# Optimization experiments

Hardware: AMD Instinct MI355X
Metric: run time of the kernel (lower is better)

Reference implementation:

```python
import jax, jax.numpy as jnp
import numpy as np

N = 100000      # nodes
E = 1600000     # edges
F_IN = 128
H = 128
L = 3           # GraphConv layers
C = 47          # classes
EPS = 1e-5      # BatchNorm eps


def setup_inputs() -> dict:
    key = jax.random.key(0)
    ks = jax.random.split(key, 12)
    feat = jax.random.normal(ks[0], (N, F_IN), dtype=jnp.float32)
    src = jax.random.randint(ks[1], (E,), 0, N, dtype=jnp.int32)
    dst = jax.random.randint(ks[2], (E,), 0, N, dtype=jnp.int32)
    s = 0.02
    W_in = jax.random.normal(ks[3], (F_IN, H), dtype=jnp.float32) * s
    b_in = jnp.zeros((H,), dtype=jnp.float32)
    Wc = jax.random.normal(ks[4], (L, H, H), dtype=jnp.float32) * s
    bc = jnp.zeros((L, H), dtype=jnp.float32)
    # BatchNorm (eval mode) params for layers+1 norms
    gamma = jnp.ones((L + 1, H), dtype=jnp.float32)
    beta = jnp.zeros((L + 1, H), dtype=jnp.float32)
    rmean = jax.random.normal(ks[5], (L + 1, H), dtype=jnp.float32) * 0.1
    rvar = jax.random.uniform(ks[6], (L + 1, H), dtype=jnp.float32, minval=0.5, maxval=1.5)
    W_out = jax.random.normal(ks[7], (H, C), dtype=jnp.float32) * s
    b_out = jnp.zeros((C,), dtype=jnp.float32)
    return {"feat": feat, "src": src, "dst": dst, "W_in": W_in, "b_in": b_in,
            "Wc": Wc, "bc": bc, "gamma": gamma, "beta": beta,
            "rmean": rmean, "rvar": rvar, "W_out": W_out, "b_out": b_out}


def _bn(x, g, b, m, v):
    # BatchNorm1d in eval mode (running stats)
    return (x - m) * jax.lax.rsqrt(v + EPS) * g + b


def _degree_norms(src, dst):
    ones = jnp.ones((E,), dtype=jnp.float32)
    deg_out = jax.ops.segment_sum(ones, src, num_segments=N)
    deg_in = jax.ops.segment_sum(ones, dst, num_segments=N)
    norm_src = jax.lax.rsqrt(jnp.maximum(deg_out, 1.0))
    norm_dst = jax.lax.rsqrt(jnp.maximum(deg_in, 1.0))
    return norm_src, norm_dst


def _graph_conv(h, src, dst, norm_src, norm_dst, W, b):
    # DGL GraphConv, norm='both': D_dst^{-1/2} A D_src^{-1/2} H W + b
    h = h * norm_src[:, None]
    agg = jax.ops.segment_sum(h[src], dst, num_segments=N)  # [N, H]
    agg = agg * norm_dst[:, None]
    return agg @ W + b


def reference(feat, src, dst, W_in, b_in, Wc, bc, gamma, beta, rmean, rvar, W_out, b_out):
    norm_src, norm_dst = _degree_norms(src, dst)
    h = feat @ W_in + b_in
    h = jax.nn.relu(_bn(h, gamma[0], beta[0], rmean[0], rvar[0]))
    # dropout is identity in eval mode
    for i in range(L):
        h = _graph_conv(h, src, dst, norm_src, norm_dst, Wc[i], bc[i])
        h = jax.nn.relu(_bn(h, gamma[i + 1], beta[i + 1], rmean[i + 1], rvar[i + 1]))
    return h @ W_out + b_out
```

## Files before the change

### kernel.cpp

```cpp
#include <hip/hip_runtime.h>
#include <cstddef>
#include <cstdint>

#define NN 100000
#define NE 1600000
#define HD 128
#define C_OUT 47
#define EPS_BN 1e-5f
#define SLAB 64
#define NXCD 8
#define GEMM0_BLOCKS ((NN + 127) / 128)
#define BUILD_BLOCKS (NE / 256)

typedef _Float16 f16;
typedef __attribute__((ext_vector_type(2))) _Float16 f16x2;
typedef __attribute__((ext_vector_type(8))) _Float16 f16x8;
typedef __attribute__((ext_vector_type(4))) float f32x4;

__device__ inline ushort f16bits(f16 h) { return __builtin_bit_cast(ushort, h); }
__device__ inline uint packf16(f16 a, f16 b) {
  return (uint)f16bits(a) | ((uint)f16bits(b) << 16);
}
__device__ inline uint xcc_id() {
  uint x;
  asm volatile("s_getreg_b32 %0, hwreg(HW_REG_XCC_ID)" : "=s"(x));
  return x & (NXCD - 1);
}

__global__ __launch_bounds__(256) void k_wsplit(
    const float* __restrict__ W_in, const float* __restrict__ Wc,
    const float* __restrict__ W_out,
    uint* __restrict__ wsHi, uint* __restrict__ wsLo) {
  int g = blockIdx.x * 256 + threadIdx.x;
  int m = g >> 13;
  int i = g & 8191;
  int kp = i >> 7, c = i & 127;
  int k = kp << 1;
  int s = kp >> 2, t = kp & 3;
  if (m < 4) {
    const float* W = (m == 0) ? W_in : (Wc + (size_t)(m - 1) * HD * HD);
    float w0 = W[(size_t)k * 128 + c];
    float w1 = W[(size_t)(k + 1) * 128 + c];
    f16 h0 = (f16)w0, h1 = (f16)w1;
    f16 l0 = (f16)(w0 - (float)h0), l1 = (f16)(w1 - (float)h1);
    int idx = m * 8192 + (s * 128 + c) * 4 + t;
    wsHi[idx] = packf16(h0, h1);
    wsLo[idx] = packf16(l0, l1);
  } else if (c < 48) {
    float w0 = (c < C_OUT) ? W_out[(size_t)k * C_OUT + c] : 0.f;
    float w1 = (c < C_OUT) ? W_out[(size_t)(k + 1) * C_OUT + c] : 0.f;
    f16 h0 = (f16)w0, h1 = (f16)w1;
    f16 l0 = (f16)(w0 - (float)h0), l1 = (f16)(w1 - (float)h1);
    int idx = 4 * 8192 + (s * 48 + c) * 4 + t;
    wsHi[idx] = packf16(h0, h1);
    wsLo[idx] = packf16(l0, l1);
  }
}

template <bool A16>
__device__ inline void gemm_body(
    const void* __restrict__ Av, const uint* __restrict__ wHi,
    const uint* __restrict__ wLo, const float* __restrict__ bias,
    const float* __restrict__ gamma, const float* __restrict__ beta,
    const float* __restrict__ rmean, const float* __restrict__ rvar,
    f16* __restrict__ out, int bx) {
  int tid = threadIdx.x;
  int wv = tid >> 6, lane = tid & 63;
  int q = lane >> 4, m16 = lane & 15;
  int row_base = bx * 128 + wv * 32;

  f32x4 acc[2][8];
  #pragma unroll
  for (int mt = 0; mt < 2; ++mt)
    #pragma unroll
    for (int nt = 0; nt < 8; ++nt)
      acc[mt][nt] = (f32x4){0.f, 0.f, 0.f, 0.f};

  #pragma unroll
  for (int kk = 0; kk < 4; ++kk) {
    f16x8 a[2];
    #pragma unroll
    for (int mt = 0; mt < 2; ++mt) {
      int r = row_base + mt * 16 + m16;
      r = r < NN ? r : NN - 1;
      if constexpr (A16) {
        a[mt] = *(const f16x8*)((const f16*)Av + (size_t)r * 128 + kk * 32 + q * 8);
      } else {
        const float4* ap = (const float4*)((const float*)Av + (size_t)r * 128 + kk * 32 + q * 8);
        float4 a0 = ap[0], a1 = ap[1];
        a[mt][0] = (f16)a0.x; a[mt][1] = (f16)a0.y;
        a[mt][2] = (f16)a0.z; a[mt][3] = (f16)a0.w;
        a[mt][4] = (f16)a1.x; a[mt][5] = (f16)a1.y;
        a[mt][6] = (f16)a1.z; a[mt][7] = (f16)a1.w;
      }
    }
    int s = kk * 4 + q;
    #pragma unroll
    for (int nt = 0; nt < 8; ++nt) {
      int n = nt * 16 + m16;
      const f16x8 whi = *(const f16x8*)&wHi[(s * 128 + n) * 4];
      const f16x8 wlo = *(const f16x8*)&wLo[(s * 128 + n) * 4];
      #pragma unroll
      for (int mt = 0; mt < 2; ++mt) {
        acc[mt][nt] = __builtin_amdgcn_mfma_f32_16x16x32_f16(a[mt], whi, acc[mt][nt], 0, 0, 0);
        acc[mt][nt] = __builtin_amdgcn_mfma_f32_16x16x32_f16(a[mt], wlo, acc[mt][nt], 0, 0, 0);
      }
    }
  }

  float s8[8], t8[8];
  #pragma unroll
  for (int nt = 0; nt < 8; ++nt) {
    int col = nt * 16 + m16;
    float sc = gamma[col] * rsqrtf(rvar[col] + EPS_BN);
    s8[nt] = sc;
    t8[nt] = (bias[col] - rmean[col]) * sc + beta[col];
  }
  #pragma unroll
  for (int mt = 0; mt < 2; ++mt) {
    #pragma unroll
    for (int nt = 0; nt < 8; ++nt) {
      int col = nt * 16 + m16;
      #pragma unroll
      for (int e = 0; e < 4; ++e) {
        int r = row_base + mt * 16 + q * 4 + e;
        if (r < NN) {
          float y = fmaxf(acc[mt][nt][e] * s8[nt] + t8[nt], 0.f);
          out[(size_t)r * 128 + col] = (f16)y;
        }
      }
    }
  }
}

__global__ __launch_bounds__(256, 4) void k_mega(
    const int* __restrict__ src, const int* __restrict__ dst,
    int* __restrict__ deg_out_c, int* __restrict__ cursor,
    int* __restrict__ slab,
    const float* __restrict__ feat, const uint* __restrict__ wsHi,
    const uint* __restrict__ wsLo, const float* __restrict__ b_in,
    const float* __restrict__ gamma, const float* __restrict__ beta,
    const float* __restrict__ rmean, const float* __restrict__ rvar,
    f16* __restrict__ h) {
  if (blockIdx.x >= GEMM0_BLOCKS) {
    int e = (blockIdx.x - GEMM0_BLOCKS) * 256 + threadIdx.x;
    if (e >= NE) return;
    int s = src[e], v = dst[e];
    uint xc = xcc_id();
    __hip_atomic_fetch_add(&deg_out_c[xc * NN + s], 1, __ATOMIC_RELAXED,
                           __HIP_MEMORY_SCOPE_WORKGROUP);
    int pos = atomicAdd(&cursor[v], 1);
    if (pos < SLAB) slab[(size_t)v * SLAB + pos] = s;
    return;
  }
  gemm_body<false>(feat, wsHi, wsLo, b_in, gamma, beta, rmean, rvar, h,
                   blockIdx.x);
}

__global__ __launch_bounds__(256) void k_norms(
    const int* __restrict__ deg_out_c, const int* __restrict__ cursor,
    float* __restrict__ norm_src, float* __restrict__ norm_dst) {
  int v = blockIdx.x * blockDim.x + threadIdx.x;
  if (v >= NN) return;
  int d = 0;
  #pragma unroll
  for (int c = 0; c < NXCD; ++c) d += deg_out_c[c * NN + v];
  norm_src[v] = rsqrtf((float)(d > 0 ? d : 1));
  int di = cursor[v];
  norm_dst[v] = rsqrtf((float)(di > 0 ? di : 1));
}

__global__ __launch_bounds__(256) void k_aggregate(
    const f16* __restrict__ h, const int* __restrict__ cursor,
    const int* __restrict__ slab, const float* __restrict__ norm_src,
    const float* __restrict__ norm_dst, f16* __restrict__ agg) {
  int wave = (int)((blockIdx.x * (unsigned)blockDim.x + threadIdx.x) >> 6);
  int lane = threadIdx.x & 63;
  if (wave >= NN) return;
  const f16x2* h2 = (const f16x2*)h;
  const int* cols = slab + (size_t)wave * SLAB;
  int d = cursor[wave];
  d = d < SLAB ? d : SLAB;
  float ax = 0.f, ay = 0.f;
  int j = 0;
  for (; j + 4 <= d; j += 4) {
    int u0 = cols[j + 0];
    int u1 = cols[j + 1];
    int u2 = cols[j + 2];
    int u3 = cols[j + 3];
    float w0 = norm_src[u0], w1 = norm_src[u1];
    float w2 = norm_src[u2], w3 = norm_src[u3];
    f16x2 x0 = h2[(size_t)u0 * 64 + lane];
    f16x2 x1 = h2[(size_t)u1 * 64 + lane];
    f16x2 x2 = h2[(size_t)u2 * 64 + lane];
    f16x2 x3 = h2[(size_t)u3 * 64 + lane];
    ax = fmaf(w0, (float)x0[0], ax); ay = fmaf(w0, (float)x0[1], ay);
    ax = fmaf(w1, (float)x1[0], ax); ay = fmaf(w1, (float)x1[1], ay);
    ax = fmaf(w2, (float)x2[0], ax); ay = fmaf(w2, (float)x2[1], ay);
    ax = fmaf(w3, (float)x3[0], ax); ay = fmaf(w3, (float)x3[1], ay);
  }
  for (; j < d; ++j) {
    int u = cols[j];
    float w = norm_src[u];
    f16x2 x = h2[(size_t)u * 64 + lane];
    ax = fmaf(w, (float)x[0], ax);
    ay = fmaf(w, (float)x[1], ay);
  }
  float nd = norm_dst[wave];
  f16x2 o;
  o[0] = (f16)(ax * nd);
  o[1] = (f16)(ay * nd);
  ((f16x2*)agg)[(size_t)wave * 64 + lane] = o;
}

__global__ __launch_bounds__(256, 4) void k_gemm(
    const f16* __restrict__ A, const uint* __restrict__ wHi,
    const uint* __restrict__ wLo, const float* __restrict__ bias,
    const float* __restrict__ gamma, const float* __restrict__ beta,
    const float* __restrict__ rmean, const float* __restrict__ rvar,
    f16* __restrict__ out) {
  gemm_body<true>(A, wHi, wLo, bias, gamma, beta, rmean, rvar, out, blockIdx.x);
}

__global__ __launch_bounds__(256, 4) void k_gemm_out(
    const f16* __restrict__ A, const uint* __restrict__ wHi,
    const uint* __restrict__ wLo, const float* __restrict__ bias,
    float* __restrict__ out) {
  int tid = threadIdx.x;
  int wv = tid >> 6, lane = tid & 63;
  int q = lane >> 4, m16 = lane & 15;
  int row_base = blockIdx.x * 128 + wv * 32;

  f32x4 acc[2][3];
  #pragma unroll
  for (int mt = 0; mt < 2; ++mt)
    #pragma unroll
    for (int nt = 0; nt < 3; ++nt)
      acc[mt][nt] = (f32x4){0.f, 0.f, 0.f, 0.f};

  #pragma unroll
  for (int kk = 0; kk < 4; ++kk) {
    f16x8 a[2];
    #pragma unroll
    for (int mt = 0; mt < 2; ++mt) {
      int r = row_base + mt * 16 + m16;
      r = r < NN ? r : NN - 1;
      a[mt] = *(const f16x8*)(A + (size_t)r * 128 + kk * 32 + q * 8);
    }
    int s = kk * 4 + q;
    #pragma unroll
    for (int nt = 0; nt < 3; ++nt) {
      int n = nt * 16 + m16;
      const f16x8 whi = *(const f16x8*)&wHi[(s * 48 + n) * 4];
      const f16x8 wlo = *(const f16x8*)&wLo[(s * 48 + n) * 4];
      #pragma unroll
      for (int mt = 0; mt < 2; ++mt) {
        acc[mt][nt] = __builtin_amdgcn_mfma_f32_16x16x32_f16(a[mt], whi, acc[mt][nt], 0, 0, 0);
        acc[mt][nt] = __builtin_amdgcn_mfma_f32_16x16x32_f16(a[mt], wlo, acc[mt][nt], 0, 0, 0);
      }
    }
  }

  #pragma unroll
  for (int nt = 0; nt < 3; ++nt) {
    int col = nt * 16 + m16;
    float b = (col < C_OUT) ? bias[col] : 0.f;
    #pragma unroll
    for (int mt = 0; mt < 2; ++mt) {
      #pragma unroll
      for (int e = 0; e < 4; ++e) {
        int r = row_base + mt * 16 + q * 4 + e;
        if (r < NN && col < C_OUT) {
          out[(size_t)r * C_OUT + col] = acc[mt][nt][e] + b;
        }
      }
    }
  }
}


extern "C" void kernel_launch(void* const* d_in, const int* in_sizes, int n_in,
                              void* d_out, int out_size, void* d_ws, size_t ws_size,
                              hipStream_t stream) {
  const float* feat = (const float*)d_in[0];
  const int* src = (const int*)d_in[1];
  const int* dst = (const int*)d_in[2];
  const float* W_in = (const float*)d_in[3];
  const float* b_in = (const float*)d_in[4];
  const float* Wc = (const float*)d_in[5];
  const float* bc = (const float*)d_in[6];
  const float* gamma = (const float*)d_in[7];
  const float* beta = (const float*)d_in[8];
  const float* rmean = (const float*)d_in[9];
  const float* rvar = (const float*)d_in[10];
  const float* W_out = (const float*)d_in[11];
  const float* b_out = (const float*)d_in[12];
  float* out = (float*)d_out;

  char* p = (char*)d_ws;
  f16* h = (f16*)p;             p += (size_t)NN * HD * sizeof(f16);
  f16* agg = (f16*)p;           p += (size_t)NN * HD * sizeof(f16);
  int* slab = (int*)p;          p += (size_t)NN * SLAB * sizeof(int);
  float* norm_src = (float*)p;  p += (size_t)NN * sizeof(float);
  float* norm_dst = (float*)p;  p += (size_t)NN * sizeof(float);
  uint* wsHi = (uint*)p;        p += (size_t)5 * 8192 * sizeof(uint);
  uint* wsLo = (uint*)p;        p += (size_t)5 * 8192 * sizeof(uint);
  int* deg_out_c = (int*)p;     p += (size_t)NXCD * NN * sizeof(int);
  int* cursor = (int*)p;        p += (size_t)NN * sizeof(int);

  hipMemsetAsync(deg_out_c, 0, (size_t)(NXCD + 1) * NN * sizeof(int), stream);

  k_wsplit<<<160, 256, 0, stream>>>(W_in, Wc, W_out, wsHi, wsLo);
  k_mega<<<GEMM0_BLOCKS + BUILD_BLOCKS, 256, 0, stream>>>(
      src, dst, deg_out_c, cursor, slab, feat, wsHi, wsLo, b_in, gamma, beta,
      rmean, rvar, h);
  k_norms<<<(NN + 255) / 256, 256, 0, stream>>>(deg_out_c, cursor, norm_src,
                                                norm_dst);

  int gblocks = (NN + 127) / 128;
  for (int l = 0; l < 3; ++l) {
    k_aggregate<<<(NN * 64 + 255) / 256, 256, 0, stream>>>(
        h, cursor, slab, norm_src, norm_dst, agg);
    k_gemm<<<gblocks, 256, 0, stream>>>(
        agg, wsHi + (size_t)(l + 1) * 8192, wsLo + (size_t)(l + 1) * 8192,
        bc + (size_t)l * HD,
        gamma + (size_t)(l + 1) * HD, beta + (size_t)(l + 1) * HD,
        rmean + (size_t)(l + 1) * HD, rvar + (size_t)(l + 1) * HD, h);
  }
  k_gemm_out<<<gblocks, 256, 0, stream>>>(
      h, wsHi + (size_t)4 * 8192, wsLo + (size_t)4 * 8192, b_out, out);
}
```

Measured before the change: 563.3 us.

## Fuse neighbor aggregation into GraphConv GEMM via LDS staging with ping-pong buffers

Replaces the separate aggregate and GEMM kernels with one kernel. Each wave gathers and normalizes neighbor features for 32 rows, two rows at a time, writes them to an LDS tile, then runs the MFMA GEMM with the fused bias, BatchNorm and ReLU epilogue. This removes the round trip of the intermediate agg tensor through global memory and one launch per layer, and double buffers h to avoid read/write hazards. In exchange, gather parallelism falls from one wave per node to one wave per 32 nodes with only 782 blocks, which may hide the latency of the random gathers less well.

```diff
diff --git a/kernel.cpp b/kernel.cpp
--- a/kernel.cpp
+++ b/kernel.cpp
@@ -11,6 +11,7 @@
 #define NXCD 8
 #define GEMM0_BLOCKS ((NN + 127) / 128)
 #define BUILD_BLOCKS (NE / 256)
+#define LDS_PITCH 136
 
 typedef _Float16 f16;
 typedef __attribute__((ext_vector_type(2))) _Float16 f16x2;
@@ -170,56 +171,130 @@
   norm_dst[v] = rsqrtf((float)(di > 0 ? di : 1));
 }
 
-__global__ __launch_bounds__(256) void k_aggregate(
-    const f16* __restrict__ h, const int* __restrict__ cursor,
+__global__ __launch_bounds__(256, 4) void k_agg_gemm(
+    const f16* __restrict__ hin, const int* __restrict__ cursor,
     const int* __restrict__ slab, const float* __restrict__ norm_src,
-    const float* __restrict__ norm_dst, f16* __restrict__ agg) {
-  int wave = (int)((blockIdx.x * (unsigned)blockDim.x + threadIdx.x) >> 6);
-  int lane = threadIdx.x & 63;
-  if (wave >= NN) return;
-  const f16x2* h2 = (const f16x2*)h;
-  const int* cols = slab + (size_t)wave * SLAB;
-  int d = cursor[wave];
-  d = d < SLAB ? d : SLAB;
-  float ax = 0.f, ay = 0.f;
-  int j = 0;
-  for (; j + 4 <= d; j += 4) {
-    int u0 = cols[j + 0];
-    int u1 = cols[j + 1];
-    int u2 = cols[j + 2];
-    int u3 = cols[j + 3];
-    float w0 = norm_src[u0], w1 = norm_src[u1];
-    float w2 = norm_src[u2], w3 = norm_src[u3];
-    f16x2 x0 = h2[(size_t)u0 * 64 + lane];
-    f16x2 x1 = h2[(size_t)u1 * 64 + lane];
-    f16x2 x2 = h2[(size_t)u2 * 64 + lane];
-    f16x2 x3 = h2[(size_t)u3 * 64 + lane];
-    ax = fmaf(w0, (float)x0[0], ax); ay = fmaf(w0, (float)x0[1], ay);
-    ax = fmaf(w1, (float)x1[0], ax); ay = fmaf(w1, (float)x1[1], ay);
-    ax = fmaf(w2, (float)x2[0], ax); ay = fmaf(w2, (float)x2[1], ay);
-    ax = fmaf(w3, (float)x3[0], ax); ay = fmaf(w3, (float)x3[1], ay);
-  }
-  for (; j < d; ++j) {
-    int u = cols[j];
-    float w = norm_src[u];
-    f16x2 x = h2[(size_t)u * 64 + lane];
-    ax = fmaf(w, (float)x[0], ax);
-    ay = fmaf(w, (float)x[1], ay);
-  }
-  float nd = norm_dst[wave];
-  f16x2 o;
-  o[0] = (f16)(ax * nd);
-  o[1] = (f16)(ay * nd);
-  ((f16x2*)agg)[(size_t)wave * 64 + lane] = o;
-}
-
-__global__ __launch_bounds__(256, 4) void k_gemm(
-    const f16* __restrict__ A, const uint* __restrict__ wHi,
-    const uint* __restrict__ wLo, const float* __restrict__ bias,
+    const float* __restrict__ norm_dst,
+    const uint* __restrict__ wHi, const uint* __restrict__ wLo,
+    const float* __restrict__ bias,
     const float* __restrict__ gamma, const float* __restrict__ beta,
     const float* __restrict__ rmean, const float* __restrict__ rvar,
-    f16* __restrict__ out) {
-  gemm_body<true>(A, wHi, wLo, bias, gamma, beta, rmean, rvar, out, blockIdx.x);
+    f16* __restrict__ hout) {
+  __shared__ f16 As[128][LDS_PITCH];
+  int tid = threadIdx.x;
+  int wv = tid >> 6, lane = tid & 63;
+  int q = lane >> 4, m16 = lane & 15;
+  int row_base = blockIdx.x * 128 + wv * 32;
+
+  const f16x2* h2 = (const f16x2*)hin;
+  for (int i = 0; i < 32; i += 2) {
+    int v0 = row_base + i, v1 = row_base + i + 1;
+    v0 = v0 < NN ? v0 : NN - 1;
+    v1 = v1 < NN ? v1 : NN - 1;
+    const int* c0 = slab + (size_t)v0 * SLAB;
+    const int* c1 = slab + (size_t)v1 * SLAB;
+    int d0 = cursor[v0]; d0 = d0 < SLAB ? d0 : SLAB;
+    int d1 = cursor[v1]; d1 = d1 < SLAB ? d1 : SLAB;
+    float a0x = 0.f, a0y = 0.f, a1x = 0.f, a1y = 0.f;
+    int dmin = d0 < d1 ? d0 : d1;
+    int j = 0;
+    for (; j + 4 <= dmin; j += 4) {
+      int u00 = c0[j], u01 = c0[j + 1], u02 = c0[j + 2], u03 = c0[j + 3];
+      int u10 = c1[j], u11 = c1[j + 1], u12 = c1[j + 2], u13 = c1[j + 3];
+      f16x2 x00 = h2[(size_t)u00 * 64 + lane];
+      f16x2 x01 = h2[(size_t)u01 * 64 + lane];
+      f16x2 x02 = h2[(size_t)u02 * 64 + lane];
+      f16x2 x03 = h2[(size_t)u03 * 64 + lane];
+      f16x2 x10 = h2[(size_t)u10 * 64 + lane];
+      f16x2 x11 = h2[(size_t)u11 * 64 + lane];
+      f16x2 x12 = h2[(size_t)u12 * 64 + lane];
+      f16x2 x13 = h2[(size_t)u13 * 64 + lane];
+      float w00 = norm_src[u00], w01 = norm_src[u01];
+      float w02 = norm_src[u02], w03 = norm_src[u03];
+      float w10 = norm_src[u10], w11 = norm_src[u11];
+      float w12 = norm_src[u12], w13 = norm_src[u13];
+      a0x = fmaf(w00, (float)x00[0], a0x); a0y = fmaf(w00, (float)x00[1], a0y);
+      a0x = fmaf(w01, (float)x01[0], a0x); a0y = fmaf(w01, (float)x01[1], a0y);
+      a0x = fmaf(w02, (float)x02[0], a0x); a0y = fmaf(w02, (float)x02[1], a0y);
+      a0x = fmaf(w03, (float)x03[0], a0x); a0y = fmaf(w03, (float)x03[1], a0y);
+      a1x = fmaf(w10, (float)x10[0], a1x); a1y = fmaf(w10, (float)x10[1], a1y);
+      a1x = fmaf(w11, (float)x11[0], a1x); a1y = fmaf(w11, (float)x11[1], a1y);
+      a1x = fmaf(w12, (float)x12[0], a1x); a1y = fmaf(w12, (float)x12[1], a1y);
+      a1x = fmaf(w13, (float)x13[0], a1x); a1y = fmaf(w13, (float)x13[1], a1y);
+    }
+    for (int t = j; t < d0; ++t) {
+      int u = c0[t];
+      float w = norm_src[u];
+      f16x2 x = h2[(size_t)u * 64 + lane];
+      a0x = fmaf(w, (float)x[0], a0x); a0y = fmaf(w, (float)x[1], a0y);
+    }
+    for (int t = j; t < d1; ++t) {
+      int u = c1[t];
+      float w = norm_src[u];
+      f16x2 x = h2[(size_t)u * 64 + lane];
+      a1x = fmaf(w, (float)x[0], a1x); a1y = fmaf(w, (float)x[1], a1y);
+    }
+    float nd0 = norm_dst[v0], nd1 = norm_dst[v1];
+    f16x2 o0, o1;
+    o0[0] = (f16)(a0x * nd0); o0[1] = (f16)(a0y * nd0);
+    o1[0] = (f16)(a1x * nd1); o1[1] = (f16)(a1y * nd1);
+    *(f16x2*)&As[wv * 32 + i][2 * lane] = o0;
+    *(f16x2*)&As[wv * 32 + i + 1][2 * lane] = o1;
+  }
+  __syncthreads();
+
+  f32x4 acc[2][8];
+  #pragma unroll
+  for (int mt = 0; mt < 2; ++mt)
+    #pragma unroll
+    for (int nt = 0; nt < 8; ++nt)
+      acc[mt][nt] = (f32x4){0.f, 0.f, 0.f, 0.f};
+
+  #pragma unroll
+  for (int kk = 0; kk < 4; ++kk) {
+    f16x8 a[2];
+    #pragma unroll
+    for (int mt = 0; mt < 2; ++mt) {
+      int lr = wv * 32 + mt * 16 + m16;
+      a[mt] = *(const f16x8*)&As[lr][kk * 32 + q * 8];
+    }
+    int s = kk * 4 + q;
+    #pragma unroll
+    for (int nt = 0; nt < 8; ++nt) {
+      int n = nt * 16 + m16;
+      const f16x8 whi = *(const f16x8*)&wHi[(s * 128 + n) * 4];
+      const f16x8 wlo = *(const f16x8*)&wLo[(s * 128 + n) * 4];
+      #pragma unroll
+      for (int mt = 0; mt < 2; ++mt) {
+        acc[mt][nt] = __builtin_amdgcn_mfma_f32_16x16x32_f16(a[mt], whi, acc[mt][nt], 0, 0, 0);
+        acc[mt][nt] = __builtin_amdgcn_mfma_f32_16x16x32_f16(a[mt], wlo, acc[mt][nt], 0, 0, 0);
+      }
+    }
+  }
+
+  float s8[8], t8[8];
+  #pragma unroll
+  for (int nt = 0; nt < 8; ++nt) {
+    int col = nt * 16 + m16;
+    float sc = gamma[col] * rsqrtf(rvar[col] + EPS_BN);
+    s8[nt] = sc;
+    t8[nt] = (bias[col] - rmean[col]) * sc + beta[col];
+  }
+  #pragma unroll
+  for (int mt = 0; mt < 2; ++mt) {
+    #pragma unroll
+    for (int nt = 0; nt < 8; ++nt) {
+      int col = nt * 16 + m16;
+      #pragma unroll
+      for (int e = 0; e < 4; ++e) {
+        int r = row_base + mt * 16 + q * 4 + e;
+        if (r < NN) {
+          float y = fmaxf(acc[mt][nt][e] * s8[nt] + t8[nt], 0.f);
+          hout[(size_t)r * 128 + col] = (f16)y;
+        }
+      }
+    }
+  }
 }
 
 __global__ __launch_bounds__(256, 4) void k_gemm_out(
@@ -298,8 +373,8 @@
   float* out = (float*)d_out;
 
   char* p = (char*)d_ws;
-  f16* h = (f16*)p;             p += (size_t)NN * HD * sizeof(f16);
-  f16* agg = (f16*)p;           p += (size_t)NN * HD * sizeof(f16);
+  f16* hA = (f16*)p;            p += (size_t)NN * HD * sizeof(f16);
+  f16* hB = (f16*)p;            p += (size_t)NN * HD * sizeof(f16);
   int* slab = (int*)p;          p += (size_t)NN * SLAB * sizeof(int);
   float* norm_src = (float*)p;  p += (size_t)NN * sizeof(float);
   float* norm_dst = (float*)p;  p += (size_t)NN * sizeof(float);
@@ -313,20 +388,22 @@
   k_wsplit<<<160, 256, 0, stream>>>(W_in, Wc, W_out, wsHi, wsLo);
   k_mega<<<GEMM0_BLOCKS + BUILD_BLOCKS, 256, 0, stream>>>(
       src, dst, deg_out_c, cursor, slab, feat, wsHi, wsLo, b_in, gamma, beta,
-      rmean, rvar, h);
+      rmean, rvar, hA);
   k_norms<<<(NN + 255) / 256, 256, 0, stream>>>(deg_out_c, cursor, norm_src,
                                                 norm_dst);
 
   int gblocks = (NN + 127) / 128;
+  f16* cur = hA;
+  f16* nxt = hB;
   for (int l = 0; l < 3; ++l) {
-    k_aggregate<<<(NN * 64 + 255) / 256, 256, 0, stream>>>(
-        h, cursor, slab, norm_src, norm_dst, agg);
-    k_gemm<<<gblocks, 256, 0, stream>>>(
-        agg, wsHi + (size_t)(l + 1) * 8192, wsLo + (size_t)(l + 1) * 8192,
+    k_agg_gemm<<<gblocks, 256, 0, stream>>>(
+        cur, cursor, slab, norm_src, norm_dst,
+        wsHi + (size_t)(l + 1) * 8192, wsLo + (size_t)(l + 1) * 8192,
         bc + (size_t)l * HD,
         gamma + (size_t)(l + 1) * HD, beta + (size_t)(l + 1) * HD,
-        rmean + (size_t)(l + 1) * HD, rvar + (size_t)(l + 1) * HD, h);
+        rmean + (size_t)(l + 1) * HD, rvar + (size_t)(l + 1) * HD, nxt);
+    f16* t = cur; cur = nxt; nxt = t;
   }
   k_gemm_out<<<gblocks, 256, 0, stream>>>(
-      h, wsHi + (size_t)4 * 8192, wsLo + (size_t)4 * 8192, b_out, out);
-}
+      cur, wsHi + (size_t)4 * 8192, wsLo + (size_t)4 * 8192, b_out, out);
+}
```

Measured after the change: 703.6 us. +24.9%, slower.

## Store features channel-chunked per XCD and aggregate with persistent work-stealing blocks

Applied to the files above, without the earlier changes.

Feature matrices h and agg move from row-major [N,128] to 8 chunks of 16 columns ([8][N][16]). The GEMMs are updated to read and write this layout. Aggregation becomes a persistent kernel of 2048 blocks in which each XCD starts on its own chunk and grabs node ranges through atomic counters, so the gathered 3.2MB chunk can stay resident in that XCD's L2. The cost is that neighbor indices are re-read 8 times (once per chunk), gathers shrink to 2-byte per-lane accesses, and atomic and barrier overhead is added.

```diff
diff --git a/kernel.cpp b/kernel.cpp
--- a/kernel.cpp
+++ b/kernel.cpp
@@ -11,6 +11,7 @@
 #define NXCD 8
 #define GEMM0_BLOCKS ((NN + 127) / 128)
 #define BUILD_BLOCKS (NE / 256)
+#define GRAB 128
 
 typedef _Float16 f16;
 typedef __attribute__((ext_vector_type(2))) _Float16 f16x2;
@@ -26,6 +27,7 @@
   asm volatile("s_getreg_b32 %0, hwreg(HW_REG_XCC_ID)" : "=s"(x));
   return x & (NXCD - 1);
 }
+
 
 __global__ __launch_bounds__(256) void k_wsplit(
     const float* __restrict__ W_in, const float* __restrict__ Wc,
@@ -84,7 +86,9 @@
       int r = row_base + mt * 16 + m16;
       r = r < NN ? r : NN - 1;
       if constexpr (A16) {
-        a[mt] = *(const f16x8*)((const f16*)Av + (size_t)r * 128 + kk * 32 + q * 8);
+        int ch = 2 * kk + (q >> 1);
+        a[mt] = *(const f16x8*)((const f16*)Av +
+                                ((size_t)ch * NN + r) * 16 + (q & 1) * 8);
       } else {
         const float4* ap = (const float4*)((const float*)Av + (size_t)r * 128 + kk * 32 + q * 8);
         float4 a0 = ap[0], a1 = ap[1];
@@ -120,13 +124,12 @@
   for (int mt = 0; mt < 2; ++mt) {
     #pragma unroll
     for (int nt = 0; nt < 8; ++nt) {
-      int col = nt * 16 + m16;
       #pragma unroll
       for (int e = 0; e < 4; ++e) {
         int r = row_base + mt * 16 + q * 4 + e;
         if (r < NN) {
           float y = fmaxf(acc[mt][nt][e] * s8[nt] + t8[nt], 0.f);
-          out[(size_t)r * 128 + col] = (f16)y;
+          out[((size_t)nt * NN + r) * 16 + m16] = (f16)y;
         }
       }
     }
@@ -170,47 +173,62 @@
   norm_dst[v] = rsqrtf((float)(di > 0 ? di : 1));
 }
 
-__global__ __launch_bounds__(256) void k_aggregate(
+__global__ __launch_bounds__(256) void k_aggregate_c(
     const f16* __restrict__ h, const int* __restrict__ cursor,
     const int* __restrict__ slab, const float* __restrict__ norm_src,
-    const float* __restrict__ norm_dst, f16* __restrict__ agg) {
-  int wave = (int)((blockIdx.x * (unsigned)blockDim.x + threadIdx.x) >> 6);
-  int lane = threadIdx.x & 63;
-  if (wave >= NN) return;
-  const f16x2* h2 = (const f16x2*)h;
-  const int* cols = slab + (size_t)wave * SLAB;
-  int d = cursor[wave];
-  d = d < SLAB ? d : SLAB;
-  float ax = 0.f, ay = 0.f;
-  int j = 0;
-  for (; j + 4 <= d; j += 4) {
-    int u0 = cols[j + 0];
-    int u1 = cols[j + 1];
-    int u2 = cols[j + 2];
-    int u3 = cols[j + 3];
-    float w0 = norm_src[u0], w1 = norm_src[u1];
-    float w2 = norm_src[u2], w3 = norm_src[u3];
-    f16x2 x0 = h2[(size_t)u0 * 64 + lane];
-    f16x2 x1 = h2[(size_t)u1 * 64 + lane];
-    f16x2 x2 = h2[(size_t)u2 * 64 + lane];
-    f16x2 x3 = h2[(size_t)u3 * 64 + lane];
-    ax = fmaf(w0, (float)x0[0], ax); ay = fmaf(w0, (float)x0[1], ay);
-    ax = fmaf(w1, (float)x1[0], ax); ay = fmaf(w1, (float)x1[1], ay);
-    ax = fmaf(w2, (float)x2[0], ax); ay = fmaf(w2, (float)x2[1], ay);
-    ax = fmaf(w3, (float)x3[0], ax); ay = fmaf(w3, (float)x3[1], ay);
-  }
-  for (; j < d; ++j) {
-    int u = cols[j];
-    float w = norm_src[u];
-    f16x2 x = h2[(size_t)u * 64 + lane];
-    ax = fmaf(w, (float)x[0], ax);
-    ay = fmaf(w, (float)x[1], ay);
-  }
-  float nd = norm_dst[wave];
-  f16x2 o;
-  o[0] = (f16)(ax * nd);
-  o[1] = (f16)(ay * nd);
-  ((f16x2*)agg)[(size_t)wave * 64 + lane] = o;
+    const float* __restrict__ norm_dst, f16* __restrict__ agg,
+    int* __restrict__ work) {
+  __shared__ int sbase;
+  int tid = threadIdx.x;
+  int lane16 = tid & 15;
+  int gid = tid >> 4;
+  uint xc = xcc_id();
+  for (int k = 0; k < NXCD; ++k) {
+    int ch = (int)((xc + k) & (NXCD - 1));
+    const f16* hc = h + (size_t)ch * NN * 16;
+    f16* ac = agg + (size_t)ch * NN * 16;
+    while (true) {
+      if (tid == 0) sbase = atomicAdd(&work[ch], GRAB);
+      __syncthreads();
+      int base = sbase;
+      __syncthreads();
+      if (base >= NN) break;
+      #pragma unroll 1
+      for (int vs = 0; vs < GRAB / 16; ++vs) {
+        int v = base + vs * 16 + gid;
+        if (v >= NN) continue;
+        int d = cursor[v];
+        d = d < SLAB ? d : SLAB;
+        const int* cols = slab + (size_t)v * SLAB;
+        float acc = 0.f;
+        int t = 0;
+        for (; t + 4 <= d; t += 4) {
+          int u0 = __builtin_nontemporal_load(cols + t + 0);
+          int u1 = __builtin_nontemporal_load(cols + t + 1);
+          int u2 = __builtin_nontemporal_load(cols + t + 2);
+          int u3 = __builtin_nontemporal_load(cols + t + 3);
+          float w0 = norm_src[u0], w1 = norm_src[u1];
+          float w2 = norm_src[u2], w3 = norm_src[u3];
+          f16 x0 = hc[(size_t)u0 * 16 + lane16];
+          f16 x1 = hc[(size_t)u1 * 16 + lane16];
+          f16 x2 = hc[(size_t)u2 * 16 + lane16];
+          f16 x3 = hc[(size_t)u3 * 16 + lane16];
+          acc = fmaf(w0, (float)x0, acc);
+          acc = fmaf(w1, (float)x1, acc);
+          acc = fmaf(w2, (float)x2, acc);
+          acc = fmaf(w3, (float)x3, acc);
+        }
+        for (; t < d; ++t) {
+          int u = __builtin_nontemporal_load(cols + t);
+          float w = norm_src[u];
+          f16 x = hc[(size_t)u * 16 + lane16];
+          acc = fmaf(w, (float)x, acc);
+        }
+        f16 o = (f16)(acc * norm_dst[v]);
+        __builtin_nontemporal_store(o, ac + (size_t)v * 16 + lane16);
+      }
+    }
+  }
 }
 
 __global__ __launch_bounds__(256, 4) void k_gemm(
@@ -245,7 +263,8 @@
     for (int mt = 0; mt < 2; ++mt) {
       int r = row_base + mt * 16 + m16;
       r = r < NN ? r : NN - 1;
-      a[mt] = *(const f16x8*)(A + (size_t)r * 128 + kk * 32 + q * 8);
+      int ch = 2 * kk + (q >> 1);
+      a[mt] = *(const f16x8*)(A + ((size_t)ch * NN + r) * 16 + (q & 1) * 8);
     }
     int s = kk * 4 + q;
     #pragma unroll
@@ -307,8 +326,10 @@
   uint* wsLo = (uint*)p;        p += (size_t)5 * 8192 * sizeof(uint);
   int* deg_out_c = (int*)p;     p += (size_t)NXCD * NN * sizeof(int);
   int* cursor = (int*)p;        p += (size_t)NN * sizeof(int);
-
-  hipMemsetAsync(deg_out_c, 0, (size_t)(NXCD + 1) * NN * sizeof(int), stream);
+  int* work = (int*)p;          p += 64 * sizeof(int);
+
+  hipMemsetAsync(deg_out_c, 0,
+                 ((size_t)(NXCD + 1) * NN + 64) * sizeof(int), stream);
 
   k_wsplit<<<160, 256, 0, stream>>>(W_in, Wc, W_out, wsHi, wsLo);
   k_mega<<<GEMM0_BLOCKS + BUILD_BLOCKS, 256, 0, stream>>>(
@@ -319,8 +340,8 @@
 
   int gblocks = (NN + 127) / 128;
   for (int l = 0; l < 3; ++l) {
-    k_aggregate<<<(NN * 64 + 255) / 256, 256, 0, stream>>>(
-        h, cursor, slab, norm_src, norm_dst, agg);
+    k_aggregate_c<<<2048, 256, 0, stream>>>(
+        h, cursor, slab, norm_src, norm_dst, agg, work + l * 8);
     k_gemm<<<gblocks, 256, 0, stream>>>(
         agg, wsHi + (size_t)(l + 1) * 8192, wsLo + (size_t)(l + 1) * 8192,
         bc + (size_t)l * HD,
```

Measured after the change: 1.636 ms. +190.5%, slower.
